# Optimization experiments

Hardware: AMD Instinct MI355X
Metric: run time of the kernel (lower is better)

The kernel has to match this reference:

```python
import jax, jax.numpy as jnp
import numpy as np

OBS, H, Z = 64, 128, 64
T, B = 512, 1024
EPS = 0.01


def _lin(x, W, b):
    # torch nn.Linear: y = x @ W.T + b, W: [out, in]
    return x @ W.T + b


def setup_inputs() -> dict:
    key = jax.random.key(0)
    ks = jax.random.split(key, 16)
    n = lambda k, shape: 0.1 * jax.random.normal(k, shape, dtype=jnp.float32)
    z = lambda shape: jnp.zeros(shape, dtype=jnp.float32)
    return {
        "s": jax.random.normal(ks[0], (T, B, OBS), dtype=jnp.float32),
        "noise": jax.random.normal(ks[1], (T, B, Z), dtype=jnp.float32),
        # phi_s / phi_z
        "W_phi_s": n(ks[2], (H, OBS)), "b_phi_s": z((H,)),
        "W_phi_z": n(ks[3], (H, Z)), "b_phi_z": z((H,)),
        # prior: Linear(H,H) ReLU Linear(H,2Z)
        "Wp1": n(ks[4], (H, H)), "bp1": z((H,)),
        "Wp2": n(ks[5], (2 * Z, H)), "bp2": z((2 * Z,)),
        # encoder: Linear(2H,H) ReLU Linear(H,2Z)
        "We1": n(ks[6], (H, 2 * H)), "be1": z((H,)),
        "We2": n(ks[7], (2 * Z, H)), "be2": z((2 * Z,)),
        # LSTMCell(input=2H, hidden=H), gate order i,f,g,o
        "W_ih": n(ks[8], (4 * H, 2 * H)), "b_ih": z((4 * H,)),
        "W_hh": n(ks[9], (4 * H, H)), "b_hh": z((4 * H,)),
        # decoder: Linear(2H,H) ReLU Linear(H,OBS)
        "Wd1": n(ks[10], (H, 2 * H)), "bd1": z((H,)),
        "Wd2": n(ks[11], (OBS, H)), "bd2": z((OBS,)),
    }


def reference(s, noise, W_phi_s, b_phi_s, W_phi_z, b_phi_z, Wp1, bp1, Wp2, bp2,
              We1, be1, We2, be2, W_ih, b_ih, W_hh, b_hh, Wd1, bd1, Wd2, bd2):
    h0 = jnp.zeros((s.shape[1], H), dtype=s.dtype)
    c0 = jnp.zeros((s.shape[1], H), dtype=s.dtype)

    def step(carry, xs):
        h, c, kl_acc, rc_acc = carry
        s_t, n_t = xs
        phi_s = _lin(s_t, W_phi_s, b_phi_s)                      # [B, H]
        # encoder on [phi_s, h]
        enc = _lin(jax.nn.relu(_lin(jnp.concatenate([phi_s, h], -1), We1, be1)), We2, be2)
        z_mu, z_std = jnp.split(enc, 2, axis=-1)
        z_std = jax.nn.softplus(z_std)
        # prior on h
        pri = _lin(jax.nn.relu(_lin(h, Wp1, bp1)), Wp2, bp2)
        p_mu, p_std = jnp.split(pri, 2, axis=-1)
        p_std = jax.nn.softplus(p_std)
        # reparameterize
        z_samp = z_mu + z_std * n_t
        phi_z = _lin(z_samp, W_phi_z, b_phi_z)                   # [B, H]
        # decode from [phi_z, h]
        recon = _lin(jax.nn.relu(_lin(jnp.concatenate([phi_z, h], -1), Wd1, bd1)), Wd2, bd2)
        # LSTM cell update with input [phi_s, phi_z]
        gates = _lin(jnp.concatenate([phi_s, phi_z], -1), W_ih, b_ih) + _lin(h, W_hh, b_hh)
        gi, gf, gg, go = jnp.split(gates, 4, axis=-1)
        c_new = jax.nn.sigmoid(gf) * c + jax.nn.sigmoid(gi) * jnp.tanh(gg)
        h_new = jax.nn.sigmoid(go) * jnp.tanh(c_new)
        # losses (sum over feature dim, mean over batch)
        rc_t = (0.5 * jnp.square(recon - s_t)).sum(-1).mean()
        kl_t = 0.5 * (2.0 * jnp.log(p_std + EPS) - 2.0 * jnp.log(z_std + EPS)
                      + (jnp.square(z_std) + jnp.square(z_mu - p_mu))
                      / (jnp.square(jnp.exp(p_std)) - 1.0)).sum(-1).mean()
        return (h_new, c_new, kl_acc + kl_t, rc_acc + rc_t), None

    (_, _, total_kl, total_rc), _ = jax.lax.scan(
        step, (h0, c0, jnp.float32(0.0), jnp.float32(0.0)), (s, noise))
    return total_kl + total_rc
```

## Files before the change

kernel.cpp:

```cpp
#include <hip/hip_runtime.h>

typedef __bf16 bf16_t;
typedef bf16_t bf16x8 __attribute__((ext_vector_type(8)));
typedef float  f32x4  __attribute__((ext_vector_type(4)));

#define TT 512
#define BB 1024

#define cL0   0
#define cL1   1024
#define cL2   3072
#define cL3   5120
#define cL4   7168
#define cL5   9216
#define cL6   10240
#define cL7   12288
#define cL8   13312
#define cL9   17408
#define cL10  21504
#define NCHUNK 29696

#define WS_FBIAS_OFF 475136
#define WS_FOLD_OFF  478208
#define WS_HSEQ_OFF  1048576
#define WS_NEED (WS_HSEQ_OFF + (size_t)TT * BB * 128 * 2)

__device__ __forceinline__ f32x4 mfma16(bf16x8 a, bf16x8 b, f32x4 c) {
  return __builtin_amdgcn_mfma_f32_16x16x32_bf16(a, b, c, 0, 0, 0);
}
__device__ __forceinline__ float sigm(float x) { return 1.0f / (1.0f + __expf(-x)); }
__device__ __forceinline__ float tanh_f(float x) {
  x = fminf(fmaxf(x, -15.0f), 15.0f);
  float e = __expf(2.0f * x);
  return (e - 1.0f) / (e + 1.0f);
}
__device__ __forceinline__ float softplus_f(float x) {
  return (x > 15.0f) ? x : __logf(1.0f + __expf(x));
}
__device__ __forceinline__ void wg_barrier() {
  asm volatile("s_waitcnt lgkmcnt(0)\n\ts_barrier" ::: "memory");
}
__device__ __forceinline__ void keep(bf16x8& v) { asm volatile("" : "+v"(v)); }

__global__ void vrnn_fold(const float* __restrict__ We1, const float* __restrict__ Wd1,
                          const float* __restrict__ Wih,
                          const float* __restrict__ Wps, const float* __restrict__ Wpz,
                          const float* __restrict__ bps, const float* __restrict__ bpz,
                          const float* __restrict__ be1, const float* __restrict__ bd1,
                          const float* __restrict__ bih, const float* __restrict__ bhh,
                          float* __restrict__ fold, float* __restrict__ fbias) {
  int id = blockIdx.x * 256 + threadIdx.x;
  if (id < 8192) {
    int n = id >> 6, k = id & 63; float acc = 0.f;
    for (int j = 0; j < 128; ++j) acc += We1[n*256 + j] * Wps[j*64 + k];
    fold[id] = acc;
  } else if (id < 16384) {
    int q = id - 8192; int n = q >> 6, k = q & 63; float acc = 0.f;
    for (int j = 0; j < 128; ++j) acc += Wd1[n*256 + j] * Wpz[j*64 + k];
    fold[id] = acc;
  } else if (id < 49152) {
    int q = id - 16384; int n = q >> 6, k = q & 63; float acc = 0.f;
    for (int j = 0; j < 128; ++j) acc += Wih[n*256 + j] * Wps[j*64 + k];
    fold[id] = acc;
  } else if (id < 81920) {
    int q = id - 49152; int n = q >> 6, k = q & 63; float acc = 0.f;
    for (int j = 0; j < 128; ++j) acc += Wih[n*256 + 128 + j] * Wpz[j*64 + k];
    fold[id] = acc;
  } else if (id < 82048) {
    int n = id - 81920; float acc = be1[n];
    for (int j = 0; j < 128; ++j) acc += We1[n*256 + j] * bps[j];
    fbias[n] = acc;
  } else if (id < 82176) {
    int n = id - 82048; float acc = bd1[n];
    for (int j = 0; j < 128; ++j) acc += Wd1[n*256 + j] * bpz[j];
    fbias[128 + n] = acc;
  } else if (id < 82688) {
    int n = id - 82176; float acc = bih[n] + bhh[n];
    for (int j = 0; j < 128; ++j) acc += Wih[n*256 + j]*bps[j] + Wih[n*256 + 128 + j]*bpz[j];
    fbias[256 + n] = acc;
  }
}

__global__ void vrnn_pack(const float* __restrict__ fold,
                          const float* __restrict__ We1, const float* __restrict__ We2,
                          const float* __restrict__ Wp1, const float* __restrict__ Wp2,
                          const float* __restrict__ Wd1, const float* __restrict__ Wd2,
                          const float* __restrict__ Whh,
                          bf16_t* __restrict__ packed) {
  int c = blockIdx.x * 256 + threadIdx.x;
  if (c >= NCHUNK) return;
  const float* src; int rs, co, Kt, base;
  if      (c < 1024)  { base = cL0;  src = fold;          rs = 64;  co = 0;   Kt = 2; }
  else if (c < 3072)  { base = cL1;  src = We1;           rs = 256; co = 128; Kt = 4; }
  else if (c < 5120)  { base = cL2;  src = We2;           rs = 128; co = 0;   Kt = 4; }
  else if (c < 7168)  { base = cL3;  src = Wp1;           rs = 128; co = 0;   Kt = 4; }
  else if (c < 9216)  { base = cL4;  src = Wp2;           rs = 128; co = 0;   Kt = 4; }
  else if (c < 10240) { base = cL5;  src = fold + 8192;   rs = 64;  co = 0;   Kt = 2; }
  else if (c < 12288) { base = cL6;  src = Wd1;           rs = 256; co = 128; Kt = 4; }
  else if (c < 13312) { base = cL7;  src = Wd2;           rs = 128; co = 0;   Kt = 4; }
  else if (c < 17408) { base = cL8;  src = fold + 16384;  rs = 64;  co = 0;   Kt = 2; }
  else if (c < 21504) { base = cL9;  src = fold + 49152;  rs = 64;  co = 0;   Kt = 2; }
  else                { base = cL10; src = Whh;           rs = 128; co = 0;   Kt = 4; }
  int local = c - base;
  int nt = local / (Kt * 64);
  int r = local - nt * Kt * 64;
  int kt = r >> 6, lane = r & 63;
  int n = nt * 16 + (lane & 15);
  int k = kt * 32 + (lane >> 4) * 8;
  const float* p = src + n * rs + co + k;
  bf16x8 v;
  #pragma unroll
  for (int j = 0; j < 8; ++j) v[j] = (bf16_t)p[j];
  *(bf16x8*)(packed + (size_t)c * 8) = v;
}

__global__ __launch_bounds__(512, 2) void vrnn_loop(
    const float* __restrict__ s, const float* __restrict__ noise,
    const bf16_t* __restrict__ packed, const float* __restrict__ fbias,
    const float* __restrict__ be2, bf16_t* __restrict__ hseq) {
  const bf16x8* Wf = (const bf16x8*)packed;

  __shared__ __align__(16) bf16_t A_h[2][16 * 136];
  __shared__ __align__(16) bf16_t A_s[2][16 * 72];
  __shared__ __align__(16) bf16_t A_z[16 * 72];
  __shared__ __align__(16) bf16_t A_e1[16 * 136];
  __shared__ __align__(16) bf16_t Wmu_lds[2048 * 8];
  __shared__ float bsm[768];

  const int tid  = threadIdx.x;
  const int wv   = tid >> 6, ln = tid & 63;
  const int quad = ln >> 4, col = ln & 15;
  const int row0 = blockIdx.x * 16;
  const int pm_  = tid >> 5;
  const int pj   = (tid & 31) * 2;
  const int nloc0 = wv * 16 + col;
  const int j_own = wv * 16 + col;
  const int wq   = wv & 3;

  for (int i = tid; i < 768; i += 512) {
    float v;
    if      (i < 128) v = fbias[i];
    else if (i < 256) v = be2[i - 128];
    else              v = fbias[256 + (i - 256)];
    bsm[i] = v;
  }
  {
    bf16x8* wl = (bf16x8*)Wmu_lds;
    for (int c = tid; c < 2048; c += 512) wl[c] = Wf[cL2 + c];
  }
  for (int i = tid; i < 16 * 136; i += 512) A_h[0][i] = (bf16_t)0.0f;
  {
    float2 v = *(const float2*)(s + ((size_t)0 * BB + row0 + pm_) * 64 + pj);
    A_s[0][pm_ * 72 + pj]     = (bf16_t)v.x;
    A_s[0][pm_ * 72 + pj + 1] = (bf16_t)v.y;
  }
  {
    unsigned long long* p = (unsigned long long*)(hseq + (size_t)row0 * 128);
    p[tid] = 0ull;
  }

  bf16x8 rb10[4][4], rb8[4][2], rb9[4][2], wE[6];
  #pragma unroll
  for (int i = 0; i < 4; ++i) {
    int nt = wv + 8 * i;
    #pragma unroll
    for (int k = 0; k < 4; ++k) { rb10[i][k] = Wf[cL10 + (nt * 4 + k) * 64 + ln]; keep(rb10[i][k]); }
    rb8[i][0] = Wf[cL8 + (nt * 2 + 0) * 64 + ln]; keep(rb8[i][0]);
    rb8[i][1] = Wf[cL8 + (nt * 2 + 1) * 64 + ln]; keep(rb8[i][1]);
    rb9[i][0] = Wf[cL9 + (nt * 2 + 0) * 64 + ln]; keep(rb9[i][0]);
    rb9[i][1] = Wf[cL9 + (nt * 2 + 1) * 64 + ln]; keep(rb9[i][1]);
  }
  wE[0] = Wf[cL0 + (wv * 2 + 0) * 64 + ln]; keep(wE[0]);
  wE[1] = Wf[cL0 + (wv * 2 + 1) * 64 + ln]; keep(wE[1]);
  #pragma unroll
  for (int k = 0; k < 4; ++k) { wE[2 + k] = Wf[cL1 + (wv * 4 + k) * 64 + ln]; keep(wE[2 + k]); }

  float nzr[4] = {0.f, 0.f, 0.f, 0.f};
  if (wv < 4) {
    #pragma unroll
    for (int r = 0; r < 4; ++r)
      nzr[r] = noise[((size_t)0 * BB + row0 + quad * 4 + r) * 64 + j_own];
  }
  float2 svN = *(const float2*)(s + ((size_t)1 * BB + row0 + pm_) * 64 + pj);

  f32x4 c_reg = {0.f, 0.f, 0.f, 0.f};
  __syncthreads();

  int cb = 0;
  for (int t = 0; t < TT; ++t) {
    const int sb = t & 1;

    bf16x8 ah0 = *(const bf16x8*)&A_h[cb][col * 136 + 0 + quad * 8];
    bf16x8 ah1 = *(const bf16x8*)&A_h[cb][col * 136 + 32 + quad * 8];
    bf16x8 ah2 = *(const bf16x8*)&A_h[cb][col * 136 + 64 + quad * 8];
    bf16x8 ah3 = *(const bf16x8*)&A_h[cb][col * 136 + 96 + quad * 8];
    bf16x8 as0 = *(const bf16x8*)&A_s[sb][col * 72 + 0 + quad * 8];
    bf16x8 as1 = *(const bf16x8*)&A_s[sb][col * 72 + 32 + quad * 8];

    {
      float bv = bsm[nloc0];
      f32x4 c = {bv, bv, bv, bv};
      c = mfma16(as0, wE[0], c);
      c = mfma16(as1, wE[1], c);
      c = mfma16(ah0, wE[2], c);
      c = mfma16(ah1, wE[3], c);
      c = mfma16(ah2, wE[4], c);
      c = mfma16(ah3, wE[5], c);
      #pragma unroll
      for (int r = 0; r < 4; ++r)
        A_e1[(quad * 4 + r) * 136 + nloc0] = (bf16_t)fmaxf(c[r], 0.0f);
    }
    f32x4 Cg[4];
    #pragma unroll
    for (int i = 0; i < 4; ++i) {
      float bv = bsm[256 + j_own + 128 * i];
      f32x4 cc = {bv, bv, bv, bv};
      cc = mfma16(ah0, rb10[i][0], cc);
      cc = mfma16(ah1, rb10[i][1], cc);
      cc = mfma16(ah2, rb10[i][2], cc);
      cc = mfma16(ah3, rb10[i][3], cc);
      cc = mfma16(as0, rb8[i][0], cc);
      cc = mfma16(as1, rb8[i][1], cc);
      Cg[i] = cc;
    }
    wg_barrier();

    {
      int lzo = 0;
      asm volatile("" : "+s"(lzo));
      const bf16x8* Wml = (const bf16x8*)Wmu_lds + lzo;
      if (wv < 4) {
        bf16x8 wmu[4], wsd[4];
        #pragma unroll
        for (int k = 0; k < 4; ++k) {
          wmu[k] = Wml[(wq * 4 + k) * 64 + ln];
          wsd[k] = Wml[((wq + 4) * 4 + k) * 64 + ln];
        }
        bf16x8 ae0 = *(const bf16x8*)&A_e1[col * 136 + 0 + quad * 8];
        bf16x8 ae1 = *(const bf16x8*)&A_e1[col * 136 + 32 + quad * 8];
        bf16x8 ae2 = *(const bf16x8*)&A_e1[col * 136 + 64 + quad * 8];
        bf16x8 ae3 = *(const bf16x8*)&A_e1[col * 136 + 96 + quad * 8];
        float bm = bsm[128 + wq * 16 + col], bs = bsm[128 + 64 + wq * 16 + col];
        f32x4 cm = {bm, bm, bm, bm};
        f32x4 cs = {bs, bs, bs, bs};
        cm = mfma16(ae0, wmu[0], cm); cs = mfma16(ae0, wsd[0], cs);
        cm = mfma16(ae1, wmu[1], cm); cs = mfma16(ae1, wsd[1], cs);
        cm = mfma16(ae2, wmu[2], cm); cs = mfma16(ae2, wsd[2], cs);
        cm = mfma16(ae3, wmu[3], cm); cs = mfma16(ae3, wsd[3], cs);
        #pragma unroll
        for (int r = 0; r < 4; ++r) {
          float z = cm[r] + softplus_f(cs[r]) * nzr[r];
          A_z[(quad * 4 + r) * 72 + wq * 16 + col] = (bf16_t)z;
        }
      }
    }
    if (t + 1 < TT) {
      A_s[sb ^ 1][pm_ * 72 + pj]     = (bf16_t)svN.x;
      A_s[sb ^ 1][pm_ * 72 + pj + 1] = (bf16_t)svN.y;
    }
    wg_barrier();

    if (wv < 4 && t + 1 < TT) {
      #pragma unroll
      for (int r = 0; r < 4; ++r)
        nzr[r] = noise[((size_t)(t + 1) * BB + row0 + quad * 4 + r) * 64 + j_own];
    }
    if (t + 2 < TT)
      svN = *(const float2*)(s + ((size_t)(t + 2) * BB + row0 + pm_) * 64 + pj);

    {
      bf16x8 az0 = *(const bf16x8*)&A_z[col * 72 + 0 + quad * 8];
      bf16x8 az1 = *(const bf16x8*)&A_z[col * 72 + 32 + quad * 8];
      #pragma unroll
      for (int i = 0; i < 4; ++i) {
        Cg[i] = mfma16(az0, rb9[i][0], Cg[i]);
        Cg[i] = mfma16(az1, rb9[i][1], Cg[i]);
      }
    }
    bf16_t* hp = hseq + (size_t)(t + 1) * BB * 128;
    #pragma unroll
    for (int r = 0; r < 4; ++r) {
      float gi = sigm(Cg[0][r]);
      float gf = sigm(Cg[1][r]);
      float gg = tanh_f(Cg[2][r]);
      float go = sigm(Cg[3][r]);
      float cn = gf * c_reg[r] + gi * gg;
      c_reg[r] = cn;
      bf16_t hv = (bf16_t)(go * tanh_f(cn));
      A_h[cb ^ 1][(quad * 4 + r) * 136 + j_own] = hv;
      if (t + 1 < TT) hp[(size_t)(row0 + quad * 4 + r) * 128 + j_own] = hv;
    }
    wg_barrier();
    cb ^= 1;
  }
}

__global__ __launch_bounds__(512, 2) void vrnn_tail(
    const float* __restrict__ s, const float* __restrict__ noise,
    const bf16_t* __restrict__ packed, const float* __restrict__ fbias,
    const float* __restrict__ bp1, const float* __restrict__ bp2,
    const float* __restrict__ be2, const float* __restrict__ bd2,
    const bf16_t* __restrict__ hseq, float* __restrict__ out) {
  const bf16x8* Wf = (const bf16x8*)packed;

  __shared__ __align__(16) bf16_t A_h[16 * 136];
  __shared__ __align__(16) bf16_t A_s[16 * 72];
  __shared__ __align__(16) bf16_t A_z[16 * 72];
  __shared__ __align__(16) bf16_t A_e1[16 * 136];
  __shared__ __align__(16) bf16_t A_p1[16 * 136];
  __shared__ __align__(16) bf16_t A_d1[16 * 136];
  __shared__ float zmu_s[16 * 68], zsd_s[16 * 68];
  __shared__ float dec2o[16 * 68];
  __shared__ float bsm[704];
  __shared__ float red[8];

  const int tid  = threadIdx.x;
  const int wv   = tid >> 6, ln = tid & 63;
  const int quad = ln >> 4, col = ln & 15;
  const int pm_  = tid >> 5;
  const int pj   = (tid & 31) * 2;
  const int nloc0 = wv * 16 + col;
  const int wq   = wv & 3;

  for (int i = tid; i < 704; i += 512) {
    float v;
    if      (i < 128) v = fbias[i];
    else if (i < 256) v = bp1[i - 128];
    else if (i < 384) v = be2[i - 256];
    else if (i < 512) v = bp2[i - 384];
    else if (i < 640) v = fbias[128 + (i - 512)];
    else              v = bd2[i - 640];
    bsm[i] = v;
  }

  bf16x8 wE[6], wP1[4], wmu[4], wsd[4], wD1[4], w5[2], w7[4];
  wE[0] = Wf[cL0 + (wv * 2 + 0) * 64 + ln];
  wE[1] = Wf[cL0 + (wv * 2 + 1) * 64 + ln];
  #pragma unroll
  for (int k = 0; k < 4; ++k) {
    wE[2 + k] = Wf[cL1 + (wv * 4 + k) * 64 + ln];
    wP1[k] = Wf[cL3 + (wv * 4 + k) * 64 + ln];
    wD1[k] = Wf[cL6 + (wv * 4 + k) * 64 + ln];
    w7[k]  = Wf[cL7 + (wq * 4 + k) * 64 + ln];
  }
  {
    int base2 = (wv < 4) ? cL2 : cL4;
    #pragma unroll
    for (int k = 0; k < 4; ++k) {
      wmu[k] = Wf[base2 + (wq * 4 + k) * 64 + ln];
      wsd[k] = Wf[base2 + ((wq + 4) * 4 + k) * 64 + ln];
    }
  }
  w5[0] = Wf[cL5 + (wv * 2 + 0) * 64 + ln];
  w5[1] = Wf[cL5 + (wv * 2 + 1) * 64 + ln];
  #pragma unroll
  for (int k = 0; k < 6; ++k) keep(wE[k]);
  #pragma unroll
  for (int k = 0; k < 4; ++k) { keep(wP1[k]); keep(wmu[k]); keep(wsd[k]); keep(wD1[k]); keep(w7[k]); }
  keep(w5[0]); keep(w5[1]);

  float kl_acc = 0.0f, rc_acc = 0.0f;
  __syncthreads();

  const int hm  = tid >> 5;
  const int hc4 = (tid & 31) * 4;

  for (int tau = blockIdx.x; tau < TT * 64; tau += gridDim.x) {
    const int t = tau >> 6;
    const int row0 = (tau & 63) * 16;

    {
      unsigned long long hv = *(const unsigned long long*)(
          hseq + (size_t)t * BB * 128 + (size_t)(row0 + hm) * 128 + hc4);
      *(unsigned long long*)&A_h[hm * 136 + hc4] = hv;
    }
    float2 sv = *(const float2*)(s + ((size_t)t * BB + row0 + pm_) * 64 + pj);
    A_s[pm_ * 72 + pj]     = (bf16_t)sv.x;
    A_s[pm_ * 72 + pj + 1] = (bf16_t)sv.y;
    float nzr[4];
    if (wv < 4) {
      #pragma unroll
      for (int r = 0; r < 4; ++r)
        nzr[r] = noise[((size_t)t * BB + row0 + quad * 4 + r) * 64 + wq * 16 + col];
    }
    wg_barrier();

    bf16x8 ah0 = *(const bf16x8*)&A_h[col * 136 + 0 + quad * 8];
    bf16x8 ah1 = *(const bf16x8*)&A_h[col * 136 + 32 + quad * 8];
    bf16x8 ah2 = *(const bf16x8*)&A_h[col * 136 + 64 + quad * 8];
    bf16x8 ah3 = *(const bf16x8*)&A_h[col * 136 + 96 + quad * 8];
    bf16x8 as0 = *(const bf16x8*)&A_s[col * 72 + 0 + quad * 8];
    bf16x8 as1 = *(const bf16x8*)&A_s[col * 72 + 32 + quad * 8];
    {
      float bv = bsm[nloc0];
      f32x4 c = {bv, bv, bv, bv};
      c = mfma16(as0, wE[0], c);
      c = mfma16(as1, wE[1], c);
      c = mfma16(ah0, wE[2], c);
      c = mfma16(ah1, wE[3], c);
      c = mfma16(ah2, wE[4], c);
      c = mfma16(ah3, wE[5], c);
      #pragma unroll
      for (int r = 0; r < 4; ++r)
        A_e1[(quad * 4 + r) * 136 + nloc0] = (bf16_t)fmaxf(c[r], 0.0f);
    }
    {
      float bv = bsm[128 + nloc0];
      f32x4 c = {bv, bv, bv, bv};
      c = mfma16(ah0, wP1[0], c);
      c = mfma16(ah1, wP1[1], c);
      c = mfma16(ah2, wP1[2], c);
      c = mfma16(ah3, wP1[3], c);
      #pragma unroll
      for (int r = 0; r < 4; ++r)
        A_p1[(quad * 4 + r) * 136 + nloc0] = (bf16_t)fmaxf(c[r], 0.0f);
    }
    wg_barrier();

    float Pmu[4], Pps[4];
    if (wv < 4) {
      bf16x8 ae0 = *(const bf16x8*)&A_e1[col * 136 + 0 + quad * 8];
      bf16x8 ae1 = *(const bf16x8*)&A_e1[col * 136 + 32 + quad * 8];
      bf16x8 ae2 = *(const bf16x8*)&A_e1[col * 136 + 64 + quad * 8];
      bf16x8 ae3 = *(const bf16x8*)&A_e1[col * 136 + 96 + quad * 8];
      float bm = bsm[256 + wq * 16 + col], bs = bsm[256 + 64 + wq * 16 + col];
      f32x4 cm = {bm, bm, bm, bm};
      f32x4 cs = {bs, bs, bs, bs};
      cm = mfma16(ae0, wmu[0], cm); cs = mfma16(ae0, wsd[0], cs);
      cm = mfma16(ae1, wmu[1], cm); cs = mfma16(ae1, wsd[1], cs);
      cm = mfma16(ae2, wmu[2], cm); cs = mfma16(ae2, wsd[2], cs);
      cm = mfma16(ae3, wmu[3], cm); cs = mfma16(ae3, wsd[3], cs);
      #pragma unroll
      for (int r = 0; r < 4; ++r) {
        float zm = cm[r];
        float zs = softplus_f(cs[r]);
        int m = quad * 4 + r;
        A_z[m * 72 + wq * 16 + col] = (bf16_t)(zm + zs * nzr[r]);
        zmu_s[m * 68 + wq * 16 + col] = zm;
        zsd_s[m * 68 + wq * 16 + col] = zs;
      }
    } else {
      bf16x8 ap0 = *(const bf16x8*)&A_p1[col * 136 + 0 + quad * 8];
      bf16x8 ap1 = *(const bf16x8*)&A_p1[col * 136 + 32 + quad * 8];
      bf16x8 ap2 = *(const bf16x8*)&A_p1[col * 136 + 64 + quad * 8];
      bf16x8 ap3 = *(const bf16x8*)&A_p1[col * 136 + 96 + quad * 8];
      float bm = bsm[384 + wq * 16 + col], bs = bsm[384 + 64 + wq * 16 + col];
      f32x4 cm = {bm, bm, bm, bm};
      f32x4 cs = {bs, bs, bs, bs};
      cm = mfma16(ap0, wmu[0], cm); cs = mfma16(ap0, wsd[0], cs);
      cm = mfma16(ap1, wmu[1], cm); cs = mfma16(ap1, wsd[1], cs);
      cm = mfma16(ap2, wmu[2], cm); cs = mfma16(ap2, wsd[2], cs);
      cm = mfma16(ap3, wmu[3], cm); cs = mfma16(ap3, wsd[3], cs);
      #pragma unroll
      for (int r = 0; r < 4; ++r) { Pmu[r] = cm[r]; Pps[r] = softplus_f(cs[r]); }
    }
    wg_barrier();

    {
      bf16x8 az0 = *(const bf16x8*)&A_z[col * 72 + 0 + quad * 8];
      bf16x8 az1 = *(const bf16x8*)&A_z[col * 72 + 32 + quad * 8];
      float bv = bsm[512 + nloc0];
      f32x4 c = {bv, bv, bv, bv};
      c = mfma16(az0, w5[0], c);
      c = mfma16(az1, w5[1], c);
      c = mfma16(ah0, wD1[0], c);
      c = mfma16(ah1, wD1[1], c);
      c = mfma16(ah2, wD1[2], c);
      c = mfma16(ah3, wD1[3], c);
      #pragma unroll
      for (int r = 0; r < 4; ++r)
        A_d1[(quad * 4 + r) * 136 + nloc0] = (bf16_t)fmaxf(c[r], 0.0f);
    }
    if (wv >= 4) {
      #pragma unroll
      for (int r = 0; r < 4; ++r) {
        int m = quad * 4 + r;
        float zm = zmu_s[m * 68 + wq * 16 + col];
        float zs = zsd_s[m * 68 + wq * 16 + col];
        float dm = zm - Pmu[r];
        float ps = Pps[r];
        float den = __expf(2.0f * ps) - 1.0f;
        kl_acc += 0.5f * (2.0f * __logf(ps + 0.01f) - 2.0f * __logf(zs + 0.01f)
                          + (zs * zs + dm * dm) / den);
      }
    }
    wg_barrier();

    if (wv >= 4) {
      bf16x8 ad0 = *(const bf16x8*)&A_d1[col * 136 + 0 + quad * 8];
      bf16x8 ad1 = *(const bf16x8*)&A_d1[col * 136 + 32 + quad * 8];
      bf16x8 ad2 = *(const bf16x8*)&A_d1[col * 136 + 64 + quad * 8];
      bf16x8 ad3 = *(const bf16x8*)&A_d1[col * 136 + 96 + quad * 8];
      float bv = bsm[640 + wq * 16 + col];
      f32x4 c = {bv, bv, bv, bv};
      c = mfma16(ad0, w7[0], c);
      c = mfma16(ad1, w7[1], c);
      c = mfma16(ad2, w7[2], c);
      c = mfma16(ad3, w7[3], c);
      #pragma unroll
      for (int r = 0; r < 4; ++r)
        dec2o[(quad * 4 + r) * 68 + wq * 16 + col] = c[r];
    }
    wg_barrier();
    {
      float d0 = dec2o[pm_ * 68 + pj] - sv.x;
      float d1 = dec2o[pm_ * 68 + pj + 1] - sv.y;
      rc_acc += 0.5f * (d0 * d0 + d1 * d1);
    }
  }

  float tot = (kl_acc + rc_acc) * (1.0f / 1024.0f);
  #pragma unroll
  for (int off = 32; off > 0; off >>= 1) tot += __shfl_down(tot, off);
  if (ln == 0) red[wv] = tot;
  __syncthreads();
  if (tid == 0) {
    float sum = 0.f;
    #pragma unroll
    for (int i = 0; i < 8; ++i) sum += red[i];
    atomicAdd(out, sum);
  }
}

__global__ __launch_bounds__(512, 2) void vrnn_mono(
    const float* __restrict__ s, const float* __restrict__ noise,
    const bf16_t* __restrict__ packed, const float* __restrict__ fbias,
    const float* __restrict__ bp1, const float* __restrict__ bp2,
    const float* __restrict__ be2, const float* __restrict__ bd2,
    float* __restrict__ out) {
  const bf16x8* Wf = (const bf16x8*)packed;
  __shared__ __align__(16) bf16_t A_h[16 * 136];
  __shared__ __align__(16) bf16_t A_s[2][16 * 72];
  __shared__ __align__(16) bf16_t A_z[16 * 72];
  __shared__ __align__(16) bf16_t A_e1[16 * 136];
  __shared__ __align__(16) bf16_t A_p1[16 * 136];
  __shared__ __align__(16) bf16_t A_d1[16 * 136];
  __shared__ float zmu_s[16 * 68], zsd_s[16 * 68];
  __shared__ float dec2o[16 * 68];
  __shared__ float bsm[1216];
  __shared__ float red[8];
  const int tid  = threadIdx.x;
  const int wv   = tid >> 6, ln = tid & 63;
  const int quad = ln >> 4, col = ln & 15;
  const int row0 = blockIdx.x * 16;
  const int pm_  = tid >> 5;
  const int pj   = (tid & 31) * 2;
  const int nloc0 = wv * 16 + col;
  const int j_own = wv * 16 + col;
  const int wq   = wv & 3;
  for (int i = tid; i < 1216; i += 512) {
    float v;
    if      (i < 128)  v = fbias[i];
    else if (i < 256)  v = bp1[i - 128];
    else if (i < 384)  v = be2[i - 256];
    else if (i < 512)  v = bp2[i - 384];
    else if (i < 640)  v = fbias[128 + (i - 512)];
    else if (i < 704)  v = bd2[i - 640];
    else               v = fbias[256 + (i - 704)];
    bsm[i] = v;
  }
  for (int i = tid; i < 16 * 136; i += 512) A_h[i] = (bf16_t)0.0f;
  {
    float2 v = *(const float2*)(s + ((size_t)0 * BB + row0 + pm_) * 64 + pj);
    A_s[0][pm_ * 72 + pj]     = (bf16_t)v.x;
    A_s[0][pm_ * 72 + pj + 1] = (bf16_t)v.y;
  }
  bf16x8 rb9[4][2], rb10[4][4];
  #pragma unroll
  for (int i = 0; i < 4; ++i) {
    int nt = wv + 8 * i;
    rb9[i][0] = Wf[cL9 + (nt * 2 + 0) * 64 + ln];
    rb9[i][1] = Wf[cL9 + (nt * 2 + 1) * 64 + ln];
    #pragma unroll
    for (int k = 0; k < 4; ++k) rb10[i][k] = Wf[cL10 + (nt * 4 + k) * 64 + ln];
  }
  bf16x8 wE0[2], wE1[4];
  wE0[0] = Wf[cL0 + (wv * 2 + 0) * 64 + ln];
  wE0[1] = Wf[cL0 + (wv * 2 + 1) * 64 + ln];
  #pragma unroll
  for (int k = 0; k < 4; ++k) wE1[k] = Wf[cL1 + (wv * 4 + k) * 64 + ln];
  bf16x8 wmu[4], wsd[4];
  {
    int base2 = (wv < 4) ? cL2 : cL4;
    #pragma unroll
    for (int k = 0; k < 4; ++k) {
      wmu[k] = Wf[base2 + (wq * 4 + k) * 64 + ln];
      wsd[k] = Wf[base2 + ((wq + 4) * 4 + k) * 64 + ln];
    }
  }
  f32x4 c_reg = {0.f, 0.f, 0.f, 0.f};
  float kl_acc = 0.0f, rc_acc = 0.0f;
  __syncthreads();
  for (int t = 0; t < TT; ++t) {
    const int sb = t & 1;
    float nzr[4];
    if (wv < 4) {
      #pragma unroll
      for (int r = 0; r < 4; ++r)
        nzr[r] = noise[((size_t)t * BB + row0 + quad * 4 + r) * 64 + j_own];
    }
    float2 svv = make_float2(0.f, 0.f);
    if (t + 1 < TT) svv = *(const float2*)(s + ((size_t)(t + 1) * BB + row0 + pm_) * 64 + pj);
    float2 spv = make_float2(0.f, 0.f);
    if (t > 0) spv = *(const float2*)(s + ((size_t)(t - 1) * BB + row0 + pm_) * 64 + pj);
    bf16x8 w8[4][2], wP1[4], wD1[4];
    #pragma unroll
    for (int i = 0; i < 4; ++i) {
      int nt = wv + 8 * i;
      w8[i][0] = Wf[cL8 + (nt * 2 + 0) * 64 + ln];
      w8[i][1] = Wf[cL8 + (nt * 2 + 1) * 64 + ln];
    }
    #pragma unroll
    for (int k = 0; k < 4; ++k) {
      wP1[k] = Wf[cL3 + (wv * 4 + k) * 64 + ln];
      wD1[k] = Wf[cL6 + (wv * 4 + k) * 64 + ln];
    }
    bf16x8 ah0 = *(const bf16x8*)&A_h[col * 136 + 0 + quad * 8];
    bf16x8 ah1 = *(const bf16x8*)&A_h[col * 136 + 32 + quad * 8];
    bf16x8 ah2 = *(const bf16x8*)&A_h[col * 136 + 64 + quad * 8];
    bf16x8 ah3 = *(const bf16x8*)&A_h[col * 136 + 96 + quad * 8];
    bf16x8 as0 = *(const bf16x8*)&A_s[sb][col * 72 + 0 + quad * 8];
    bf16x8 as1 = *(const bf16x8*)&A_s[sb][col * 72 + 32 + quad * 8];
    {
      float bv = bsm[nloc0];
      f32x4 c = {bv, bv, bv, bv};
      c = mfma16(as0, wE0[0], c);
      c = mfma16(as1, wE0[1], c);
      c = mfma16(ah0, wE1[0], c);
      c = mfma16(ah1, wE1[1], c);
      c = mfma16(ah2, wE1[2], c);
      c = mfma16(ah3, wE1[3], c);
      #pragma unroll
      for (int r = 0; r < 4; ++r)
        A_e1[(quad * 4 + r) * 136 + nloc0] = (bf16_t)fmaxf(c[r], 0.0f);
    }
    f32x4 Cg[4];
    #pragma unroll
    for (int i = 0; i < 4; ++i) {
      float bv = bsm[704 + j_own + 128 * i];
      f32x4 cc = {bv, bv, bv, bv};
      cc = mfma16(ah0, rb10[i][0], cc);
      cc = mfma16(ah1, rb10[i][1], cc);
      cc = mfma16(ah2, rb10[i][2], cc);
      cc = mfma16(ah3, rb10[i][3], cc);
      cc = mfma16(as0, w8[i][0], cc);
      cc = mfma16(as1, w8[i][1], cc);
      Cg[i] = cc;
    }
    {
      float bv = bsm[128 + nloc0];
      f32x4 c = {bv, bv, bv, bv};
      c = mfma16(ah0, wP1[0], c);
      c = mfma16(ah1, wP1[1], c);
      c = mfma16(ah2, wP1[2], c);
      c = mfma16(ah3, wP1[3], c);
      #pragma unroll
      for (int r = 0; r < 4; ++r)
        A_p1[(quad * 4 + r) * 136 + nloc0] = (bf16_t)fmaxf(c[r], 0.0f);
    }
    f32x4 Cd;
    {
      float bv = bsm[512 + nloc0];
      f32x4 c = {bv, bv, bv, bv};
      c = mfma16(ah0, wD1[0], c);
      c = mfma16(ah1, wD1[1], c);
      c = mfma16(ah2, wD1[2], c);
      c = mfma16(ah3, wD1[3], c);
      Cd = c;
    }
    if (wv >= 4 && t > 0) {
      bf16x8 ad0 = *(const bf16x8*)&A_d1[col * 136 + 0 + quad * 8];
      bf16x8 ad1 = *(const bf16x8*)&A_d1[col * 136 + 32 + quad * 8];
      bf16x8 ad2 = *(const bf16x8*)&A_d1[col * 136 + 64 + quad * 8];
      bf16x8 ad3 = *(const bf16x8*)&A_d1[col * 136 + 96 + quad * 8];
      bf16x8 w7[4];
      #pragma unroll
      for (int k = 0; k < 4; ++k) w7[k] = Wf[cL7 + (wq * 4 + k) * 64 + ln];
      float bv = bsm[640 + wq * 16 + col];
      f32x4 c = {bv, bv, bv, bv};
      c = mfma16(ad0, w7[0], c);
      c = mfma16(ad1, w7[1], c);
      c = mfma16(ad2, w7[2], c);
      c = mfma16(ad3, w7[3], c);
      #pragma unroll
      for (int r = 0; r < 4; ++r)
        dec2o[(quad * 4 + r) * 68 + wq * 16 + col] = c[r];
    }
    wg_barrier();
    float Pmu[4], Pps[4];
    if (wv < 4) {
      bf16x8 ae0 = *(const bf16x8*)&A_e1[col * 136 + 0 + quad * 8];
      bf16x8 ae1 = *(const bf16x8*)&A_e1[col * 136 + 32 + quad * 8];
      bf16x8 ae2 = *(const bf16x8*)&A_e1[col * 136 + 64 + quad * 8];
      bf16x8 ae3 = *(const bf16x8*)&A_e1[col * 136 + 96 + quad * 8];
      float bm = bsm[256 + wq * 16 + col], bs = bsm[256 + 64 + wq * 16 + col];
      f32x4 cm = {bm, bm, bm, bm};
      f32x4 cs = {bs, bs, bs, bs};
      cm = mfma16(ae0, wmu[0], cm); cs = mfma16(ae0, wsd[0], cs);
      cm = mfma16(ae1, wmu[1], cm); cs = mfma16(ae1, wsd[1], cs);
      cm = mfma16(ae2, wmu[2], cm); cs = mfma16(ae2, wsd[2], cs);
      cm = mfma16(ae3, wmu[3], cm); cs = mfma16(ae3, wsd[3], cs);
      #pragma unroll
      for (int r = 0; r < 4; ++r) {
        float zm = cm[r];
        float zs = softplus_f(cs[r]);
        float z = zm + zs * nzr[r];
        int m = quad * 4 + r;
        A_z[m * 72 + j_own] = (bf16_t)z;
        zmu_s[m * 68 + j_own] = zm;
        zsd_s[m * 68 + j_own] = zs;
      }
    } else {
      bf16x8 ap0 = *(const bf16x8*)&A_p1[col * 136 + 0 + quad * 8];
      bf16x8 ap1 = *(const bf16x8*)&A_p1[col * 136 + 32 + quad * 8];
      bf16x8 ap2 = *(const bf16x8*)&A_p1[col * 136 + 64 + quad * 8];
      bf16x8 ap3 = *(const bf16x8*)&A_p1[col * 136 + 96 + quad * 8];
      float bm = bsm[384 + wq * 16 + col], bs = bsm[384 + 64 + wq * 16 + col];
      f32x4 cm = {bm, bm, bm, bm};
      f32x4 cs = {bs, bs, bs, bs};
      cm = mfma16(ap0, wmu[0], cm); cs = mfma16(ap0, wsd[0], cs);
      cm = mfma16(ap1, wmu[1], cm); cs = mfma16(ap1, wsd[1], cs);
      cm = mfma16(ap2, wmu[2], cm); cs = mfma16(ap2, wsd[2], cs);
      cm = mfma16(ap3, wmu[3], cm); cs = mfma16(ap3, wsd[3], cs);
      #pragma unroll
      for (int r = 0; r < 4; ++r) { Pmu[r] = cm[r]; Pps[r] = softplus_f(cs[r]); }
    }
    if (t > 0) {
      float d0 = dec2o[pm_ * 68 + pj] - spv.x;
      float d1 = dec2o[pm_ * 68 + pj + 1] - spv.y;
      rc_acc += 0.5f * (d0 * d0 + d1 * d1);
    }
    if (t + 1 < TT) {
      A_s[sb ^ 1][pm_ * 72 + pj]     = (bf16_t)svv.x;
      A_s[sb ^ 1][pm_ * 72 + pj + 1] = (bf16_t)svv.y;
    }
    wg_barrier();
    bf16x8 az0 = *(const bf16x8*)&A_z[col * 72 + 0 + quad * 8];
    bf16x8 az1 = *(const bf16x8*)&A_z[col * 72 + 32 + quad * 8];
    #pragma unroll
    for (int i = 0; i < 4; ++i) {
      Cg[i] = mfma16(az0, rb9[i][0], Cg[i]);
      Cg[i] = mfma16(az1, rb9[i][1], Cg[i]);
    }
    {
      bf16x8 w5a = Wf[cL5 + (wv * 2 + 0) * 64 + ln];
      bf16x8 w5b = Wf[cL5 + (wv * 2 + 1) * 64 + ln];
      Cd = mfma16(az0, w5a, Cd);
      Cd = mfma16(az1, w5b, Cd);
      #pragma unroll
      for (int r = 0; r < 4; ++r)
        A_d1[(quad * 4 + r) * 136 + nloc0] = (bf16_t)fmaxf(Cd[r], 0.0f);
    }
    #pragma unroll
    for (int r = 0; r < 4; ++r) {
      float gi = sigm(Cg[0][r]);
      float gf = sigm(Cg[1][r]);
      float gg = tanh_f(Cg[2][r]);
      float go = sigm(Cg[3][r]);
      float cn = gf * c_reg[r] + gi * gg;
      c_reg[r] = cn;
      A_h[(quad * 4 + r) * 136 + j_own] = (bf16_t)(go * tanh_f(cn));
    }
    if (wv >= 4) {
      #pragma unroll
      for (int r = 0; r < 4; ++r) {
        int m = quad * 4 + r;
        float zm = zmu_s[m * 68 + wq * 16 + col];
        float zs = zsd_s[m * 68 + wq * 16 + col];
        float dm = zm - Pmu[r];
        float ps = Pps[r];
        float den = __expf(2.0f * ps) - 1.0f;
        kl_acc += 0.5f * (2.0f * __logf(ps + 0.01f) - 2.0f * __logf(zs + 0.01f)
                          + (zs * zs + dm * dm) / den);
      }
    }
    wg_barrier();
  }
  if (wv >= 4) {
    bf16x8 ad0 = *(const bf16x8*)&A_d1[col * 136 + 0 + quad * 8];
    bf16x8 ad1 = *(const bf16x8*)&A_d1[col * 136 + 32 + quad * 8];
    bf16x8 ad2 = *(const bf16x8*)&A_d1[col * 136 + 64 + quad * 8];
    bf16x8 ad3 = *(const bf16x8*)&A_d1[col * 136 + 96 + quad * 8];
    bf16x8 w7[4];
    #pragma unroll
    for (int k = 0; k < 4; ++k) w7[k] = Wf[cL7 + (wq * 4 + k) * 64 + ln];
    float bv = bsm[640 + wq * 16 + col];
    f32x4 c = {bv, bv, bv, bv};
    c = mfma16(ad0, w7[0], c);
    c = mfma16(ad1, w7[1], c);
    c = mfma16(ad2, w7[2], c);
    c = mfma16(ad3, w7[3], c);
    #pragma unroll
    for (int r = 0; r < 4; ++r)
      dec2o[(quad * 4 + r) * 68 + wq * 16 + col] = c[r];
  }
  __syncthreads();
  {
    float2 sl = *(const float2*)(s + ((size_t)(TT - 1) * BB + row0 + pm_) * 64 + pj);
    float d0 = dec2o[pm_ * 68 + pj] - sl.x;
    float d1 = dec2o[pm_ * 68 + pj + 1] - sl.y;
    rc_acc += 0.5f * (d0 * d0 + d1 * d1);
  }
  float tot = (kl_acc + rc_acc) * (1.0f / 1024.0f);
  #pragma unroll
  for (int off = 32; off > 0; off >>= 1) tot += __shfl_down(tot, off);
  if (ln == 0) red[wv] = tot;
  __syncthreads();
  if (tid == 0) {
    float sum = 0.f;
    #pragma unroll
    for (int i = 0; i < 8; ++i) sum += red[i];
    atomicAdd(out, sum);
  }
}

extern "C" void kernel_launch(void* const* d_in, const int* in_sizes, int n_in,
                              void* d_out, int out_size, void* d_ws, size_t ws_size,
                              hipStream_t stream) {
  (void)in_sizes; (void)n_in; (void)out_size;
  const float* s   = (const float*)d_in[0];
  const float* nz  = (const float*)d_in[1];
  const float* Wps = (const float*)d_in[2];
  const float* bps = (const float*)d_in[3];
  const float* Wpz = (const float*)d_in[4];
  const float* bpz = (const float*)d_in[5];
  const float* Wp1 = (const float*)d_in[6];
  const float* bp1 = (const float*)d_in[7];
  const float* Wp2 = (const float*)d_in[8];
  const float* bp2 = (const float*)d_in[9];
  const float* We1 = (const float*)d_in[10];
  const float* be1 = (const float*)d_in[11];
  const float* We2 = (const float*)d_in[12];
  const float* be2 = (const float*)d_in[13];
  const float* Wih = (const float*)d_in[14];
  const float* bih = (const float*)d_in[15];
  const float* Whh = (const float*)d_in[16];
  const float* bhh = (const float*)d_in[17];
  const float* Wd1 = (const float*)d_in[18];
  const float* bd1 = (const float*)d_in[19];
  const float* Wd2 = (const float*)d_in[20];
  const float* bd2 = (const float*)d_in[21];

  bf16_t* packed = (bf16_t*)d_ws;
  float* fbias = (float*)((char*)d_ws + WS_FBIAS_OFF);
  float* fold  = (float*)((char*)d_ws + WS_FOLD_OFF);
  bf16_t* hseq = (bf16_t*)((char*)d_ws + WS_HSEQ_OFF);

  hipMemsetAsync(d_out, 0, sizeof(float), stream);
  vrnn_fold<<<(82688 + 255) / 256, 256, 0, stream>>>(We1, Wd1, Wih, Wps, Wpz, bps, bpz,
                                                     be1, bd1, bih, bhh, fold, fbias);
  vrnn_pack<<<(NCHUNK + 255) / 256, 256, 0, stream>>>(fold, We1, We2, Wp1, Wp2, Wd1, Wd2,
                                                      Whh, packed);
  if (ws_size >= WS_NEED) {
    vrnn_loop<<<64, 512, 0, stream>>>(s, nz, packed, fbias, be2, hseq);
    vrnn_tail<<<256, 512, 0, stream>>>(s, nz, packed, fbias, bp1, bp2, be2, bd2, hseq,
                                       (float*)d_out);
  } else {
    vrnn_mono<<<64, 512, 0, stream>>>(s, nz, packed, fbias, bp1, bp2, be2, bd2,
                                      (float*)d_out);
  }
}
```

Before: 1.868 ms.

## Fuse recurrent loop and loss tail into single monolithic kernel with register-resident weights

Replaces the two-kernel split, a recurrent LSTM loop that writes every hidden state to a workspace followed by a parallel tail kernel that recomputes encoder, prior and decoder losses, with one kernel that does all per-step work inside the recurrence. Prior, decoder and second-layer weights are kept in registers or LDS, and the recon loss is pipelined one step late to hide the decoder's second layer. This removes the hidden-state write and reload traffic and the second launch. In exchange it adds MFMA and LDS work to the serial critical path of the 64-block recurrence, and raises register and LDS pressure.

```diff
diff --git a/kernel.cpp b/kernel.cpp
--- a/kernel.cpp
+++ b/kernel.cpp
@@ -22,8 +22,6 @@
 
 #define WS_FBIAS_OFF 475136
 #define WS_FOLD_OFF  478208
-#define WS_HSEQ_OFF  1048576
-#define WS_NEED (WS_HSEQ_OFF + (size_t)TT * BB * 128 * 2)
 
 __device__ __forceinline__ f32x4 mfma16(bf16x8 a, bf16x8 b, f32x4 c) {
   return __builtin_amdgcn_mfma_f32_16x16x32_bf16(a, b, c, 0, 0, 0);
@@ -114,18 +112,25 @@
   *(bf16x8*)(packed + (size_t)c * 8) = v;
 }
 
-__global__ __launch_bounds__(512, 2) void vrnn_loop(
+__global__ __launch_bounds__(512, 2) void vrnn_mono2(
     const float* __restrict__ s, const float* __restrict__ noise,
     const bf16_t* __restrict__ packed, const float* __restrict__ fbias,
-    const float* __restrict__ be2, bf16_t* __restrict__ hseq) {
+    const float* __restrict__ bp1, const float* __restrict__ bp2,
+    const float* __restrict__ be2, const float* __restrict__ bd2,
+    float* __restrict__ out) {
   const bf16x8* Wf = (const bf16x8*)packed;
 
   __shared__ __align__(16) bf16_t A_h[2][16 * 136];
   __shared__ __align__(16) bf16_t A_s[2][16 * 72];
   __shared__ __align__(16) bf16_t A_z[16 * 72];
   __shared__ __align__(16) bf16_t A_e1[16 * 136];
-  __shared__ __align__(16) bf16_t Wmu_lds[2048 * 8];
-  __shared__ float bsm[768];
+  __shared__ __align__(16) bf16_t A_p1[16 * 136];
+  __shared__ __align__(16) bf16_t A_d1[16 * 136];
+  __shared__ __align__(16) bf16_t Wlds[4096 * 8];
+  __shared__ float zmu_s[16 * 68], zsd_s[16 * 68];
+  __shared__ float dec2o[16 * 68];
+  __shared__ float bsm[1216];
+  __shared__ float red[8];
 
   const int tid  = threadIdx.x;
   const int wv   = tid >> 6, ln = tid & 63;
@@ -137,29 +142,25 @@
   const int j_own = wv * 16 + col;
   const int wq   = wv & 3;
 
-  for (int i = tid; i < 768; i += 512) {
+  for (int i = tid; i < 1216; i += 512) {
     float v;
-    if      (i < 128) v = fbias[i];
-    else if (i < 256) v = be2[i - 128];
-    else              v = fbias[256 + (i - 256)];
+    if      (i < 128)  v = fbias[i];
+    else if (i < 256)  v = bp1[i - 128];
+    else if (i < 384)  v = be2[i - 256];
+    else if (i < 512)  v = bp2[i - 384];
+    else if (i < 640)  v = fbias[128 + (i - 512)];
+    else if (i < 704)  v = bd2[i - 640];
+    else               v = fbias[256 + (i - 704)];
     bsm[i] = v;
   }
   {
-    bf16x8* wl = (bf16x8*)Wmu_lds;
-    for (int c = tid; c < 2048; c += 512) wl[c] = Wf[cL2 + c];
+    bf16x8* wl = (bf16x8*)Wlds;
+    for (int c = tid; c < 4096; c += 512)
+      wl[c] = Wf[(c < 2048) ? (cL2 + c) : (cL4 + (c - 2048))];
   }
   for (int i = tid; i < 16 * 136; i += 512) A_h[0][i] = (bf16_t)0.0f;
-  {
-    float2 v = *(const float2*)(s + ((size_t)0 * BB + row0 + pm_) * 64 + pj);
-    A_s[0][pm_ * 72 + pj]     = (bf16_t)v.x;
-    A_s[0][pm_ * 72 + pj + 1] = (bf16_t)v.y;
-  }
-  {
-    unsigned long long* p = (unsigned long long*)(hseq + (size_t)row0 * 128);
-    p[tid] = 0ull;
-  }
-
-  bf16x8 rb10[4][4], rb8[4][2], rb9[4][2], wE[6];
+
+  bf16x8 rb10[4][4], rb8[4][2], rb9[4][2], wE[6], wP1[4], wD1[4], w5[2], w7[4];
   #pragma unroll
   for (int i = 0; i < 4; ++i) {
     int nt = wv + 8 * i;
@@ -173,7 +174,14 @@
   wE[0] = Wf[cL0 + (wv * 2 + 0) * 64 + ln]; keep(wE[0]);
   wE[1] = Wf[cL0 + (wv * 2 + 1) * 64 + ln]; keep(wE[1]);
   #pragma unroll
-  for (int k = 0; k < 4; ++k) { wE[2 + k] = Wf[cL1 + (wv * 4 + k) * 64 + ln]; keep(wE[2 + k]); }
+  for (int k = 0; k < 4; ++k) {
+    wE[2 + k] = Wf[cL1 + (wv * 4 + k) * 64 + ln]; keep(wE[2 + k]);
+    wP1[k] = Wf[cL3 + (wv * 4 + k) * 64 + ln]; keep(wP1[k]);
+    wD1[k] = Wf[cL6 + (wv * 4 + k) * 64 + ln]; keep(wD1[k]);
+    w7[k]  = Wf[cL7 + (wq * 4 + k) * 64 + ln]; keep(w7[k]);
+  }
+  w5[0] = Wf[cL5 + (wv * 2 + 0) * 64 + ln]; keep(w5[0]);
+  w5[1] = Wf[cL5 + (wv * 2 + 1) * 64 + ln]; keep(w5[1]);
 
   float nzr[4] = {0.f, 0.f, 0.f, 0.f};
   if (wv < 4) {
@@ -181,9 +189,16 @@
     for (int r = 0; r < 4; ++r)
       nzr[r] = noise[((size_t)0 * BB + row0 + quad * 4 + r) * 64 + j_own];
   }
+  float2 sP0 = *(const float2*)(s + ((size_t)0 * BB + row0 + pm_) * 64 + pj);
   float2 svN = *(const float2*)(s + ((size_t)1 * BB + row0 + pm_) * 64 + pj);
+  float2 sPm1 = make_float2(0.f, 0.f);
+  {
+    A_s[0][pm_ * 72 + pj]     = (bf16_t)sP0.x;
+    A_s[0][pm_ * 72 + pj + 1] = (bf16_t)sP0.y;
+  }
 
   f32x4 c_reg = {0.f, 0.f, 0.f, 0.f};
+  float kl_acc = 0.0f, rc_acc = 0.0f;
   __syncthreads();
 
   int cb = 0;
@@ -210,10 +225,31 @@
       for (int r = 0; r < 4; ++r)
         A_e1[(quad * 4 + r) * 136 + nloc0] = (bf16_t)fmaxf(c[r], 0.0f);
     }
+    {
+      float bv = bsm[128 + nloc0];
+      f32x4 c = {bv, bv, bv, bv};
+      c = mfma16(ah0, wP1[0], c);
+      c = mfma16(ah1, wP1[1], c);
+      c = mfma16(ah2, wP1[2], c);
+      c = mfma16(ah3, wP1[3], c);
+      #pragma unroll
+      for (int r = 0; r < 4; ++r)
+        A_p1[(quad * 4 + r) * 136 + nloc0] = (bf16_t)fmaxf(c[r], 0.0f);
+    }
+    f32x4 Cd;
+    {
+      float bv = bsm[512 + nloc0];
+      f32x4 c = {bv, bv, bv, bv};
+      c = mfma16(ah0, wD1[0], c);
+      c = mfma16(ah1, wD1[1], c);
+      c = mfma16(ah2, wD1[2], c);
+      c = mfma16(ah3, wD1[3], c);
+      Cd = c;
+    }
     f32x4 Cg[4];
     #pragma unroll
     for (int i = 0; i < 4; ++i) {
-      float bv = bsm[256 + j_own + 128 * i];
+      float bv = bsm[704 + j_own + 128 * i];
       f32x4 cc = {bv, bv, bv, bv};
       cc = mfma16(ah0, rb10[i][0], cc);
       cc = mfma16(ah1, rb10[i][1], cc);
@@ -223,24 +259,40 @@
       cc = mfma16(as1, rb8[i][1], cc);
       Cg[i] = cc;
     }
+    if (wv >= 4 && t > 0) {
+      bf16x8 ad0 = *(const bf16x8*)&A_d1[col * 136 + 0 + quad * 8];
+      bf16x8 ad1 = *(const bf16x8*)&A_d1[col * 136 + 32 + quad * 8];
+      bf16x8 ad2 = *(const bf16x8*)&A_d1[col * 136 + 64 + quad * 8];
+      bf16x8 ad3 = *(const bf16x8*)&A_d1[col * 136 + 96 + quad * 8];
+      float bv = bsm[640 + wq * 16 + col];
+      f32x4 c = {bv, bv, bv, bv};
+      c = mfma16(ad0, w7[0], c);
+      c = mfma16(ad1, w7[1], c);
+      c = mfma16(ad2, w7[2], c);
+      c = mfma16(ad3, w7[3], c);
+      #pragma unroll
+      for (int r = 0; r < 4; ++r)
+        dec2o[(quad * 4 + r) * 68 + wq * 16 + col] = c[r];
+    }
     wg_barrier();
 
+    float Pmu[4], Pps[4];
     {
       int lzo = 0;
       asm volatile("" : "+s"(lzo));
-      const bf16x8* Wml = (const bf16x8*)Wmu_lds + lzo;
+      const bf16x8* Wml = (const bf16x8*)Wlds + ((wv < 4) ? 0 : 2048) + lzo;
+      bf16x8 wmu[4], wsd[4];
+      #pragma unroll
+      for (int k = 0; k < 4; ++k) {
+        wmu[k] = Wml[(wq * 4 + k) * 64 + ln];
+        wsd[k] = Wml[((wq + 4) * 4 + k) * 64 + ln];
+      }
       if (wv < 4) {
-        bf16x8 wmu[4], wsd[4];
-        #pragma unroll
-        for (int k = 0; k < 4; ++k) {
-          wmu[k] = Wml[(wq * 4 + k) * 64 + ln];
-          wsd[k] = Wml[((wq + 4) * 4 + k) * 64 + ln];
-        }
         bf16x8 ae0 = *(const bf16x8*)&A_e1[col * 136 + 0 + quad * 8];
         bf16x8 ae1 = *(const bf16x8*)&A_e1[col * 136 + 32 + quad * 8];
         bf16x8 ae2 = *(const bf16x8*)&A_e1[col * 136 + 64 + quad * 8];
         bf16x8 ae3 = *(const bf16x8*)&A_e1[col * 136 + 96 + quad * 8];
-        float bm = bsm[128 + wq * 16 + col], bs = bsm[128 + 64 + wq * 16 + col];
+        float bm = bsm[256 + wq * 16 + col], bs = bsm[256 + 64 + wq * 16 + col];
         f32x4 cm = {bm, bm, bm, bm};
         f32x4 cs = {bs, bs, bs, bs};
         cm = mfma16(ae0, wmu[0], cm); cs = mfma16(ae0, wsd[0], cs);
@@ -249,15 +301,40 @@
         cm = mfma16(ae3, wmu[3], cm); cs = mfma16(ae3, wsd[3], cs);
         #pragma unroll
         for (int r = 0; r < 4; ++r) {
-          float z = cm[r] + softplus_f(cs[r]) * nzr[r];
-          A_z[(quad * 4 + r) * 72 + wq * 16 + col] = (bf16_t)z;
+          float zm = cm[r];
+          float zs = softplus_f(cs[r]);
+          int m = quad * 4 + r;
+          A_z[m * 72 + wq * 16 + col] = (bf16_t)(zm + zs * nzr[r]);
+          zmu_s[m * 68 + wq * 16 + col] = zm;
+          zsd_s[m * 68 + wq * 16 + col] = zs;
         }
+      } else {
+        bf16x8 ap0 = *(const bf16x8*)&A_p1[col * 136 + 0 + quad * 8];
+        bf16x8 ap1 = *(const bf16x8*)&A_p1[col * 136 + 32 + quad * 8];
+        bf16x8 ap2 = *(const bf16x8*)&A_p1[col * 136 + 64 + quad * 8];
+        bf16x8 ap3 = *(const bf16x8*)&A_p1[col * 136 + 96 + quad * 8];
+        float bm = bsm[384 + wq * 16 + col], bs = bsm[384 + 64 + wq * 16 + col];
+        f32x4 cm = {bm, bm, bm, bm};
+        f32x4 cs = {bs, bs, bs, bs};
+        cm = mfma16(ap0, wmu[0], cm); cs = mfma16(ap0, wsd[0], cs);
+        cm = mfma16(ap1, wmu[1], cm); cs = mfma16(ap1, wsd[1], cs);
+        cm = mfma16(ap2, wmu[2], cm); cs = mfma16(ap2, wsd[2], cs);
+        cm = mfma16(ap3, wmu[3], cm); cs = mfma16(ap3, wsd[3], cs);
+        #pragma unroll
+        for (int r = 0; r < 4; ++r) { Pmu[r] = cm[r]; Pps[r] = softplus_f(cs[r]); }
       }
+    }
+    if (t > 0) {
+      float d0 = dec2o[pm_ * 68 + pj] - sPm1.x;
+      float d1 = dec2o[pm_ * 68 + pj + 1] - sPm1.y;
+      rc_acc += 0.5f * (d0 * d0 + d1 * d1);
     }
     if (t + 1 < TT) {
       A_s[sb ^ 1][pm_ * 72 + pj]     = (bf16_t)svN.x;
       A_s[sb ^ 1][pm_ * 72 + pj + 1] = (bf16_t)svN.y;
     }
+    sPm1 = sP0;
+    sP0 = svN;
     wg_barrier();
 
     if (wv < 4 && t + 1 < TT) {
@@ -276,8 +353,12 @@
         Cg[i] = mfma16(az0, rb9[i][0], Cg[i]);
         Cg[i] = mfma16(az1, rb9[i][1], Cg[i]);
       }
-    }
-    bf16_t* hp = hseq + (size_t)(t + 1) * BB * 128;
+      Cd = mfma16(az0, w5[0], Cd);
+      Cd = mfma16(az1, w5[1], Cd);
+      #pragma unroll
+      for (int r = 0; r < 4; ++r)
+        A_d1[(quad * 4 + r) * 136 + nloc0] = (bf16_t)fmaxf(Cd[r], 0.0f);
+    }
     #pragma unroll
     for (int r = 0; r < 4; ++r) {
       float gi = sigm(Cg[0][r]);
@@ -286,190 +367,7 @@
       float go = sigm(Cg[3][r]);
       float cn = gf * c_reg[r] + gi * gg;
       c_reg[r] = cn;
-      bf16_t hv = (bf16_t)(go * tanh_f(cn));
-      A_h[cb ^ 1][(quad * 4 + r) * 136 + j_own] = hv;
-      if (t + 1 < TT) hp[(size_t)(row0 + quad * 4 + r) * 128 + j_own] = hv;
-    }
-    wg_barrier();
-    cb ^= 1;
-  }
-}
-
-__global__ __launch_bounds__(512, 2) void vrnn_tail(
-    const float* __restrict__ s, const float* __restrict__ noise,
-    const bf16_t* __restrict__ packed, const float* __restrict__ fbias,
-    const float* __restrict__ bp1, const float* __restrict__ bp2,
-    const float* __restrict__ be2, const float* __restrict__ bd2,
-    const bf16_t* __restrict__ hseq, float* __restrict__ out) {
-  const bf16x8* Wf = (const bf16x8*)packed;
-
-  __shared__ __align__(16) bf16_t A_h[16 * 136];
-  __shared__ __align__(16) bf16_t A_s[16 * 72];
-  __shared__ __align__(16) bf16_t A_z[16 * 72];
-  __shared__ __align__(16) bf16_t A_e1[16 * 136];
-  __shared__ __align__(16) bf16_t A_p1[16 * 136];
-  __shared__ __align__(16) bf16_t A_d1[16 * 136];
-  __shared__ float zmu_s[16 * 68], zsd_s[16 * 68];
-  __shared__ float dec2o[16 * 68];
-  __shared__ float bsm[704];
-  __shared__ float red[8];
-
-  const int tid  = threadIdx.x;
-  const int wv   = tid >> 6, ln = tid & 63;
-  const int quad = ln >> 4, col = ln & 15;
-  const int pm_  = tid >> 5;
-  const int pj   = (tid & 31) * 2;
-  const int nloc0 = wv * 16 + col;
-  const int wq   = wv & 3;
-
-  for (int i = tid; i < 704; i += 512) {
-    float v;
-    if      (i < 128) v = fbias[i];
-    else if (i < 256) v = bp1[i - 128];
-    else if (i < 384) v = be2[i - 256];
-    else if (i < 512) v = bp2[i - 384];
-    else if (i < 640) v = fbias[128 + (i - 512)];
-    else              v = bd2[i - 640];
-    bsm[i] = v;
-  }
-
-  bf16x8 wE[6], wP1[4], wmu[4], wsd[4], wD1[4], w5[2], w7[4];
-  wE[0] = Wf[cL0 + (wv * 2 + 0) * 64 + ln];
-  wE[1] = Wf[cL0 + (wv * 2 + 1) * 64 + ln];
-  #pragma unroll
-  for (int k = 0; k < 4; ++k) {
-    wE[2 + k] = Wf[cL1 + (wv * 4 + k) * 64 + ln];
-    wP1[k] = Wf[cL3 + (wv * 4 + k) * 64 + ln];
-    wD1[k] = Wf[cL6 + (wv * 4 + k) * 64 + ln];
-    w7[k]  = Wf[cL7 + (wq * 4 + k) * 64 + ln];
-  }
-  {
-    int base2 = (wv < 4) ? cL2 : cL4;
-    #pragma unroll
-    for (int k = 0; k < 4; ++k) {
-      wmu[k] = Wf[base2 + (wq * 4 + k) * 64 + ln];
-      wsd[k] = Wf[base2 + ((wq + 4) * 4 + k) * 64 + ln];
-    }
-  }
-  w5[0] = Wf[cL5 + (wv * 2 + 0) * 64 + ln];
-  w5[1] = Wf[cL5 + (wv * 2 + 1) * 64 + ln];
-  #pragma unroll
-  for (int k = 0; k < 6; ++k) keep(wE[k]);
-  #pragma unroll
-  for (int k = 0; k < 4; ++k) { keep(wP1[k]); keep(wmu[k]); keep(wsd[k]); keep(wD1[k]); keep(w7[k]); }
-  keep(w5[0]); keep(w5[1]);
-
-  float kl_acc = 0.0f, rc_acc = 0.0f;
-  __syncthreads();
-
-  const int hm  = tid >> 5;
-  const int hc4 = (tid & 31) * 4;
-
-  for (int tau = blockIdx.x; tau < TT * 64; tau += gridDim.x) {
-    const int t = tau >> 6;
-    const int row0 = (tau & 63) * 16;
-
-    {
-      unsigned long long hv = *(const unsigned long long*)(
-          hseq + (size_t)t * BB * 128 + (size_t)(row0 + hm) * 128 + hc4);
-      *(unsigned long long*)&A_h[hm * 136 + hc4] = hv;
-    }
-    float2 sv = *(const float2*)(s + ((size_t)t * BB + row0 + pm_) * 64 + pj);
-    A_s[pm_ * 72 + pj]     = (bf16_t)sv.x;
-    A_s[pm_ * 72 + pj + 1] = (bf16_t)sv.y;
-    float nzr[4];
-    if (wv < 4) {
-      #pragma unroll
-      for (int r = 0; r < 4; ++r)
-        nzr[r] = noise[((size_t)t * BB + row0 + quad * 4 + r) * 64 + wq * 16 + col];
-    }
-    wg_barrier();
-
-    bf16x8 ah0 = *(const bf16x8*)&A_h[col * 136 + 0 + quad * 8];
-    bf16x8 ah1 = *(const bf16x8*)&A_h[col * 136 + 32 + quad * 8];
-    bf16x8 ah2 = *(const bf16x8*)&A_h[col * 136 + 64 + quad * 8];
-    bf16x8 ah3 = *(const bf16x8*)&A_h[col * 136 + 96 + quad * 8];
-    bf16x8 as0 = *(const bf16x8*)&A_s[col * 72 + 0 + quad * 8];
-    bf16x8 as1 = *(const bf16x8*)&A_s[col * 72 + 32 + quad * 8];
-    {
-      float bv = bsm[nloc0];
-      f32x4 c = {bv, bv, bv, bv};
-      c = mfma16(as0, wE[0], c);
-      c = mfma16(as1, wE[1], c);
-      c = mfma16(ah0, wE[2], c);
-      c = mfma16(ah1, wE[3], c);
-      c = mfma16(ah2, wE[4], c);
-      c = mfma16(ah3, wE[5], c);
-      #pragma unroll
-      for (int r = 0; r < 4; ++r)
-        A_e1[(quad * 4 + r) * 136 + nloc0] = (bf16_t)fmaxf(c[r], 0.0f);
-    }
-    {
-      float bv = bsm[128 + nloc0];
-      f32x4 c = {bv, bv, bv, bv};
-      c = mfma16(ah0, wP1[0], c);
-      c = mfma16(ah1, wP1[1], c);
-      c = mfma16(ah2, wP1[2], c);
-      c = mfma16(ah3, wP1[3], c);
-      #pragma unroll
-      for (int r = 0; r < 4; ++r)
-        A_p1[(quad * 4 + r) * 136 + nloc0] = (bf16_t)fmaxf(c[r], 0.0f);
-    }
-    wg_barrier();
-
-    float Pmu[4], Pps[4];
-    if (wv < 4) {
-      bf16x8 ae0 = *(const bf16x8*)&A_e1[col * 136 + 0 + quad * 8];
-      bf16x8 ae1 = *(const bf16x8*)&A_e1[col * 136 + 32 + quad * 8];
-      bf16x8 ae2 = *(const bf16x8*)&A_e1[col * 136 + 64 + quad * 8];
-      bf16x8 ae3 = *(const bf16x8*)&A_e1[col * 136 + 96 + quad * 8];
-      float bm = bsm[256 + wq * 16 + col], bs = bsm[256 + 64 + wq * 16 + col];
-      f32x4 cm = {bm, bm, bm, bm};
-      f32x4 cs = {bs, bs, bs, bs};
-      cm = mfma16(ae0, wmu[0], cm); cs = mfma16(ae0, wsd[0], cs);
-      cm = mfma16(ae1, wmu[1], cm); cs = mfma16(ae1, wsd[1], cs);
-      cm = mfma16(ae2, wmu[2], cm); cs = mfma16(ae2, wsd[2], cs);
-      cm = mfma16(ae3, wmu[3], cm); cs = mfma16(ae3, wsd[3], cs);
-      #pragma unroll
-      for (int r = 0; r < 4; ++r) {
-        float zm = cm[r];
-        float zs = softplus_f(cs[r]);
-        int m = quad * 4 + r;
-        A_z[m * 72 + wq * 16 + col] = (bf16_t)(zm + zs * nzr[r]);
-        zmu_s[m * 68 + wq * 16 + col] = zm;
-        zsd_s[m * 68 + wq * 16 + col] = zs;
-      }
-    } else {
-      bf16x8 ap0 = *(const bf16x8*)&A_p1[col * 136 + 0 + quad * 8];
-      bf16x8 ap1 = *(const bf16x8*)&A_p1[col * 136 + 32 + quad * 8];
-      bf16x8 ap2 = *(const bf16x8*)&A_p1[col * 136 + 64 + quad * 8];
-      bf16x8 ap3 = *(const bf16x8*)&A_p1[col * 136 + 96 + quad * 8];
-      float bm = bsm[384 + wq * 16 + col], bs = bsm[384 + 64 + wq * 16 + col];
-      f32x4 cm = {bm, bm, bm, bm};
-      f32x4 cs = {bs, bs, bs, bs};
-      cm = mfma16(ap0, wmu[0], cm); cs = mfma16(ap0, wsd[0], cs);
-      cm = mfma16(ap1, wmu[1], cm); cs = mfma16(ap1, wsd[1], cs);
-      cm = mfma16(ap2, wmu[2], cm); cs = mfma16(ap2, wsd[2], cs);
-      cm = mfma16(ap3, wmu[3], cm); cs = mfma16(ap3, wsd[3], cs);
-      #pragma unroll
-      for (int r = 0; r < 4; ++r) { Pmu[r] = cm[r]; Pps[r] = softplus_f(cs[r]); }
-    }
-    wg_barrier();
-
-    {
-      bf16x8 az0 = *(const bf16x8*)&A_z[col * 72 + 0 + quad * 8];
-      bf16x8 az1 = *(const bf16x8*)&A_z[col * 72 + 32 + quad * 8];
-      float bv = bsm[512 + nloc0];
-      f32x4 c = {bv, bv, bv, bv};
-      c = mfma16(az0, w5[0], c);
-      c = mfma16(az1, w5[1], c);
-      c = mfma16(ah0, wD1[0], c);
-      c = mfma16(ah1, wD1[1], c);
-      c = mfma16(ah2, wD1[2], c);
-      c = mfma16(ah3, wD1[3], c);
-      #pragma unroll
-      for (int r = 0; r < 4; ++r)
-        A_d1[(quad * 4 + r) * 136 + nloc0] = (bf16_t)fmaxf(c[r], 0.0f);
+      A_h[cb ^ 1][(quad * 4 + r) * 136 + j_own] = (bf16_t)(go * tanh_f(cn));
     }
     if (wv >= 4) {
       #pragma unroll
@@ -485,28 +383,29 @@
       }
     }
     wg_barrier();
-
-    if (wv >= 4) {
-      bf16x8 ad0 = *(const bf16x8*)&A_d1[col * 136 + 0 + quad * 8];
-      bf16x8 ad1 = *(const bf16x8*)&A_d1[col * 136 + 32 + quad * 8];
-      bf16x8 ad2 = *(const bf16x8*)&A_d1[col * 136 + 64 + quad * 8];
-      bf16x8 ad3 = *(const bf16x8*)&A_d1[col * 136 + 96 + quad * 8];
-      float bv = bsm[640 + wq * 16 + col];
-      f32x4 c = {bv, bv, bv, bv};
-      c = mfma16(ad0, w7[0], c);
-      c = mfma16(ad1, w7[1], c);
-      c = mfma16(ad2, w7[2], c);
-      c = mfma16(ad3, w7[3], c);
-      #pragma unroll
-      for (int r = 0; r < 4; ++r)
-        dec2o[(quad * 4 + r) * 68 + wq * 16 + col] = c[r];
-    }
-    wg_barrier();
-    {
-      float d0 = dec2o[pm_ * 68 + pj] - sv.x;
-      float d1 = dec2o[pm_ * 68 + pj + 1] - sv.y;
-      rc_acc += 0.5f * (d0 * d0 + d1 * d1);
-    }
+    cb ^= 1;
+  }
+
+  if (wv >= 4) {
+    bf16x8 ad0 = *(const bf16x8*)&A_d1[col * 136 + 0 + quad * 8];
+    bf16x8 ad1 = *(const bf16x8*)&A_d1[col * 136 + 32 + quad * 8];
+    bf16x8 ad2 = *(const bf16x8*)&A_d1[col * 136 + 64 + quad * 8];
+    bf16x8 ad3 = *(const bf16x8*)&A_d1[col * 136 + 96 + quad * 8];
+    float bv = bsm[640 + wq * 16 + col];
+    f32x4 c = {bv, bv, bv, bv};
+    c = mfma16(ad0, w7[0], c);
+    c = mfma16(ad1, w7[1], c);
+    c = mfma16(ad2, w7[2], c);
+    c = mfma16(ad3, w7[3], c);
+    #pragma unroll
+    for (int r = 0; r < 4; ++r)
+      dec2o[(quad * 4 + r) * 68 + wq * 16 + col] = c[r];
+  }
+  wg_barrier();
+  {
+    float d0 = dec2o[pm_ * 68 + pj] - sPm1.x;
+    float d1 = dec2o[pm_ * 68 + pj + 1] - sPm1.y;
+    rc_acc += 0.5f * (d0 * d0 + d1 * d1);
   }
 
   float tot = (kl_acc + rc_acc) * (1.0f / 1024.0f);
@@ -522,302 +421,10 @@
   }
 }
 
-__global__ __launch_bounds__(512, 2) void vrnn_mono(
-    const float* __restrict__ s, const float* __restrict__ noise,
-    const bf16_t* __restrict__ packed, const float* __restrict__ fbias,
-    const float* __restrict__ bp1, const float* __restrict__ bp2,
-    const float* __restrict__ be2, const float* __restrict__ bd2,
-    float* __restrict__ out) {
-  const bf16x8* Wf = (const bf16x8*)packed;
-  __shared__ __align__(16) bf16_t A_h[16 * 136];
-  __shared__ __align__(16) bf16_t A_s[2][16 * 72];
-  __shared__ __align__(16) bf16_t A_z[16 * 72];
-  __shared__ __align__(16) bf16_t A_e1[16 * 136];
-  __shared__ __align__(16) bf16_t A_p1[16 * 136];
-  __shared__ __align__(16) bf16_t A_d1[16 * 136];
-  __shared__ float zmu_s[16 * 68], zsd_s[16 * 68];
-  __shared__ float dec2o[16 * 68];
-  __shared__ float bsm[1216];
-  __shared__ float red[8];
-  const int tid  = threadIdx.x;
-  const int wv   = tid >> 6, ln = tid & 63;
-  const int quad = ln >> 4, col = ln & 15;
-  const int row0 = blockIdx.x * 16;
-  const int pm_  = tid >> 5;
-  const int pj   = (tid & 31) * 2;
-  const int nloc0 = wv * 16 + col;
-  const int j_own = wv * 16 + col;
-  const int wq   = wv & 3;
-  for (int i = tid; i < 1216; i += 512) {
-    float v;
-    if      (i < 128)  v = fbias[i];
-    else if (i < 256)  v = bp1[i - 128];
-    else if (i < 384)  v = be2[i - 256];
-    else if (i < 512)  v = bp2[i - 384];
-    else if (i < 640)  v = fbias[128 + (i - 512)];
-    else if (i < 704)  v = bd2[i - 640];
-    else               v = fbias[256 + (i - 704)];
-    bsm[i] = v;
-  }
-  for (int i = tid; i < 16 * 136; i += 512) A_h[i] = (bf16_t)0.0f;
-  {
-    float2 v = *(const float2*)(s + ((size_t)0 * BB + row0 + pm_) * 64 + pj);
-    A_s[0][pm_ * 72 + pj]     = (bf16_t)v.x;
-    A_s[0][pm_ * 72 + pj + 1] = (bf16_t)v.y;
-  }
-  bf16x8 rb9[4][2], rb10[4][4];
-  #pragma unroll
-  for (int i = 0; i < 4; ++i) {
-    int nt = wv + 8 * i;
-    rb9[i][0] = Wf[cL9 + (nt * 2 + 0) * 64 + ln];
-    rb9[i][1] = Wf[cL9 + (nt * 2 + 1) * 64 + ln];
-    #pragma unroll
-    for (int k = 0; k < 4; ++k) rb10[i][k] = Wf[cL10 + (nt * 4 + k) * 64 + ln];
-  }
-  bf16x8 wE0[2], wE1[4];
-  wE0[0] = Wf[cL0 + (wv * 2 + 0) * 64 + ln];
-  wE0[1] = Wf[cL0 + (wv * 2 + 1) * 64 + ln];
-  #pragma unroll
-  for (int k = 0; k < 4; ++k) wE1[k] = Wf[cL1 + (wv * 4 + k) * 64 + ln];
-  bf16x8 wmu[4], wsd[4];
-  {
-    int base2 = (wv < 4) ? cL2 : cL4;
-    #pragma unroll
-    for (int k = 0; k < 4; ++k) {
-      wmu[k] = Wf[base2 + (wq * 4 + k) * 64 + ln];
-      wsd[k] = Wf[base2 + ((wq + 4) * 4 + k) * 64 + ln];
-    }
-  }
-  f32x4 c_reg = {0.f, 0.f, 0.f, 0.f};
-  float kl_acc = 0.0f, rc_acc = 0.0f;
-  __syncthreads();
-  for (int t = 0; t < TT; ++t) {
-    const int sb = t & 1;
-    float nzr[4];
-    if (wv < 4) {
-      #pragma unroll
-      for (int r = 0; r < 4; ++r)
-        nzr[r] = noise[((size_t)t * BB + row0 + quad * 4 + r) * 64 + j_own];
-    }
-    float2 svv = make_float2(0.f, 0.f);
-    if (t + 1 < TT) svv = *(const float2*)(s + ((size_t)(t + 1) * BB + row0 + pm_) * 64 + pj);
-    float2 spv = make_float2(0.f, 0.f);
-    if (t > 0) spv = *(const float2*)(s + ((size_t)(t - 1) * BB + row0 + pm_) * 64 + pj);
-    bf16x8 w8[4][2], wP1[4], wD1[4];
-    #pragma unroll
-    for (int i = 0; i < 4; ++i) {
-      int nt = wv + 8 * i;
-      w8[i][0] = Wf[cL8 + (nt * 2 + 0) * 64 + ln];
-      w8[i][1] = Wf[cL8 + (nt * 2 + 1) * 64 + ln];
-    }
-    #pragma unroll
-    for (int k = 0; k < 4; ++k) {
-      wP1[k] = Wf[cL3 + (wv * 4 + k) * 64 + ln];
-      wD1[k] = Wf[cL6 + (wv * 4 + k) * 64 + ln];
-    }
-    bf16x8 ah0 = *(const bf16x8*)&A_h[col * 136 + 0 + quad * 8];
-    bf16x8 ah1 = *(const bf16x8*)&A_h[col * 136 + 32 + quad * 8];
-    bf16x8 ah2 = *(const bf16x8*)&A_h[col * 136 + 64 + quad * 8];
-    bf16x8 ah3 = *(const bf16x8*)&A_h[col * 136 + 96 + quad * 8];
-    bf16x8 as0 = *(const bf16x8*)&A_s[sb][col * 72 + 0 + quad * 8];
-    bf16x8 as1 = *(const bf16x8*)&A_s[sb][col * 72 + 32 + quad * 8];
-    {
-      float bv = bsm[nloc0];
-      f32x4 c = {bv, bv, bv, bv};
-      c = mfma16(as0, wE0[0], c);
-      c = mfma16(as1, wE0[1], c);
-      c = mfma16(ah0, wE1[0], c);
-      c = mfma16(ah1, wE1[1], c);
-      c = mfma16(ah2, wE1[2], c);
-      c = mfma16(ah3, wE1[3], c);
-      #pragma unroll
-      for (int r = 0; r < 4; ++r)
-        A_e1[(quad * 4 + r) * 136 + nloc0] = (bf16_t)fmaxf(c[r], 0.0f);
-    }
-    f32x4 Cg[4];
-    #pragma unroll
-    for (int i = 0; i < 4; ++i) {
-      float bv = bsm[704 + j_own + 128 * i];
-      f32x4 cc = {bv, bv, bv, bv};
-      cc = mfma16(ah0, rb10[i][0], cc);
-      cc = mfma16(ah1, rb10[i][1], cc);
-      cc = mfma16(ah2, rb10[i][2], cc);
-      cc = mfma16(ah3, rb10[i][3], cc);
-      cc = mfma16(as0, w8[i][0], cc);
-      cc = mfma16(as1, w8[i][1], cc);
-      Cg[i] = cc;
-    }
-    {
-      float bv = bsm[128 + nloc0];
-      f32x4 c = {bv, bv, bv, bv};
-      c = mfma16(ah0, wP1[0], c);
-      c = mfma16(ah1, wP1[1], c);
-      c = mfma16(ah2, wP1[2], c);
-      c = mfma16(ah3, wP1[3], c);
-      #pragma unroll
-      for (int r = 0; r < 4; ++r)
-        A_p1[(quad * 4 + r) * 136 + nloc0] = (bf16_t)fmaxf(c[r], 0.0f);
-    }
-    f32x4 Cd;
-    {
-      float bv = bsm[512 + nloc0];
-      f32x4 c = {bv, bv, bv, bv};
-      c = mfma16(ah0, wD1[0], c);
-      c = mfma16(ah1, wD1[1], c);
-      c = mfma16(ah2, wD1[2], c);
-      c = mfma16(ah3, wD1[3], c);
-      Cd = c;
-    }
-    if (wv >= 4 && t > 0) {
-      bf16x8 ad0 = *(const bf16x8*)&A_d1[col * 136 + 0 + quad * 8];
-      bf16x8 ad1 = *(const bf16x8*)&A_d1[col * 136 + 32 + quad * 8];
-      bf16x8 ad2 = *(const bf16x8*)&A_d1[col * 136 + 64 + quad * 8];
-      bf16x8 ad3 = *(const bf16x8*)&A_d1[col * 136 + 96 + quad * 8];
-      bf16x8 w7[4];
-      #pragma unroll
-      for (int k = 0; k < 4; ++k) w7[k] = Wf[cL7 + (wq * 4 + k) * 64 + ln];
-      float bv = bsm[640 + wq * 16 + col];
-      f32x4 c = {bv, bv, bv, bv};
-      c = mfma16(ad0, w7[0], c);
-      c = mfma16(ad1, w7[1], c);
-      c = mfma16(ad2, w7[2], c);
-      c = mfma16(ad3, w7[3], c);
-      #pragma unroll
-      for (int r = 0; r < 4; ++r)
-        dec2o[(quad * 4 + r) * 68 + wq * 16 + col] = c[r];
-    }
-    wg_barrier();
-    float Pmu[4], Pps[4];
-    if (wv < 4) {
-      bf16x8 ae0 = *(const bf16x8*)&A_e1[col * 136 + 0 + quad * 8];
-      bf16x8 ae1 = *(const bf16x8*)&A_e1[col * 136 + 32 + quad * 8];
-      bf16x8 ae2 = *(const bf16x8*)&A_e1[col * 136 + 64 + quad * 8];
-      bf16x8 ae3 = *(const bf16x8*)&A_e1[col * 136 + 96 + quad * 8];
-      float bm = bsm[256 + wq * 16 + col], bs = bsm[256 + 64 + wq * 16 + col];
-      f32x4 cm = {bm, bm, bm, bm};
-      f32x4 cs = {bs, bs, bs, bs};
-      cm = mfma16(ae0, wmu[0], cm); cs = mfma16(ae0, wsd[0], cs);
-      cm = mfma16(ae1, wmu[1], cm); cs = mfma16(ae1, wsd[1], cs);
-      cm = mfma16(ae2, wmu[2], cm); cs = mfma16(ae2, wsd[2], cs);
-      cm = mfma16(ae3, wmu[3], cm); cs = mfma16(ae3, wsd[3], cs);
-      #pragma unroll
-      for (int r = 0; r < 4; ++r) {
-        float zm = cm[r];
-        float zs = softplus_f(cs[r]);
-        float z = zm + zs * nzr[r];
-        int m = quad * 4 + r;
-        A_z[m * 72 + j_own] = (bf16_t)z;
-        zmu_s[m * 68 + j_own] = zm;
-        zsd_s[m * 68 + j_own] = zs;
-      }
-    } else {
-      bf16x8 ap0 = *(const bf16x8*)&A_p1[col * 136 + 0 + quad * 8];
-      bf16x8 ap1 = *(const bf16x8*)&A_p1[col * 136 + 32 + quad * 8];
-      bf16x8 ap2 = *(const bf16x8*)&A_p1[col * 136 + 64 + quad * 8];
-      bf16x8 ap3 = *(const bf16x8*)&A_p1[col * 136 + 96 + quad * 8];
-      float bm = bsm[384 + wq * 16 + col], bs = bsm[384 + 64 + wq * 16 + col];
-      f32x4 cm = {bm, bm, bm, bm};
-      f32x4 cs = {bs, bs, bs, bs};
-      cm = mfma16(ap0, wmu[0], cm); cs = mfma16(ap0, wsd[0], cs);
-      cm = mfma16(ap1, wmu[1], cm); cs = mfma16(ap1, wsd[1], cs);
-      cm = mfma16(ap2, wmu[2], cm); cs = mfma16(ap2, wsd[2], cs);
-      cm = mfma16(ap3, wmu[3], cm); cs = mfma16(ap3, wsd[3], cs);
-      #pragma unroll
-      for (int r = 0; r < 4; ++r) { Pmu[r] = cm[r]; Pps[r] = softplus_f(cs[r]); }
-    }
-    if (t > 0) {
-      float d0 = dec2o[pm_ * 68 + pj] - spv.x;
-      float d1 = dec2o[pm_ * 68 + pj + 1] - spv.y;
-      rc_acc += 0.5f * (d0 * d0 + d1 * d1);
-    }
-    if (t + 1 < TT) {
-      A_s[sb ^ 1][pm_ * 72 + pj]     = (bf16_t)svv.x;
-      A_s[sb ^ 1][pm_ * 72 + pj + 1] = (bf16_t)svv.y;
-    }
-    wg_barrier();
-    bf16x8 az0 = *(const bf16x8*)&A_z[col * 72 + 0 + quad * 8];
-    bf16x8 az1 = *(const bf16x8*)&A_z[col * 72 + 32 + quad * 8];
-    #pragma unroll
-    for (int i = 0; i < 4; ++i) {
-      Cg[i] = mfma16(az0, rb9[i][0], Cg[i]);
-      Cg[i] = mfma16(az1, rb9[i][1], Cg[i]);
-    }
-    {
-      bf16x8 w5a = Wf[cL5 + (wv * 2 + 0) * 64 + ln];
-      bf16x8 w5b = Wf[cL5 + (wv * 2 + 1) * 64 + ln];
-      Cd = mfma16(az0, w5a, Cd);
-      Cd = mfma16(az1, w5b, Cd);
-      #pragma unroll
-      for (int r = 0; r < 4; ++r)
-        A_d1[(quad * 4 + r) * 136 + nloc0] = (bf16_t)fmaxf(Cd[r], 0.0f);
-    }
-    #pragma unroll
-    for (int r = 0; r < 4; ++r) {
-      float gi = sigm(Cg[0][r]);
-      float gf = sigm(Cg[1][r]);
-      float gg = tanh_f(Cg[2][r]);
-      float go = sigm(Cg[3][r]);
-      float cn = gf * c_reg[r] + gi * gg;
-      c_reg[r] = cn;
-      A_h[(quad * 4 + r) * 136 + j_own] = (bf16_t)(go * tanh_f(cn));
-    }
-    if (wv >= 4) {
-      #pragma unroll
-      for (int r = 0; r < 4; ++r) {
-        int m = quad * 4 + r;
-        float zm = zmu_s[m * 68 + wq * 16 + col];
-        float zs = zsd_s[m * 68 + wq * 16 + col];
-        float dm = zm - Pmu[r];
-        float ps = Pps[r];
-        float den = __expf(2.0f * ps) - 1.0f;
-        kl_acc += 0.5f * (2.0f * __logf(ps + 0.01f) - 2.0f * __logf(zs + 0.01f)
-                          + (zs * zs + dm * dm) / den);
-      }
-    }
-    wg_barrier();
-  }
-  if (wv >= 4) {
-    bf16x8 ad0 = *(const bf16x8*)&A_d1[col * 136 + 0 + quad * 8];
-    bf16x8 ad1 = *(const bf16x8*)&A_d1[col * 136 + 32 + quad * 8];
-    bf16x8 ad2 = *(const bf16x8*)&A_d1[col * 136 + 64 + quad * 8];
-    bf16x8 ad3 = *(const bf16x8*)&A_d1[col * 136 + 96 + quad * 8];
-    bf16x8 w7[4];
-    #pragma unroll
-    for (int k = 0; k < 4; ++k) w7[k] = Wf[cL7 + (wq * 4 + k) * 64 + ln];
-    float bv = bsm[640 + wq * 16 + col];
-    f32x4 c = {bv, bv, bv, bv};
-    c = mfma16(ad0, w7[0], c);
-    c = mfma16(ad1, w7[1], c);
-    c = mfma16(ad2, w7[2], c);
-    c = mfma16(ad3, w7[3], c);
-    #pragma unroll
-    for (int r = 0; r < 4; ++r)
-      dec2o[(quad * 4 + r) * 68 + wq * 16 + col] = c[r];
-  }
-  __syncthreads();
-  {
-    float2 sl = *(const float2*)(s + ((size_t)(TT - 1) * BB + row0 + pm_) * 64 + pj);
-    float d0 = dec2o[pm_ * 68 + pj] - sl.x;
-    float d1 = dec2o[pm_ * 68 + pj + 1] - sl.y;
-    rc_acc += 0.5f * (d0 * d0 + d1 * d1);
-  }
-  float tot = (kl_acc + rc_acc) * (1.0f / 1024.0f);
-  #pragma unroll
-  for (int off = 32; off > 0; off >>= 1) tot += __shfl_down(tot, off);
-  if (ln == 0) red[wv] = tot;
-  __syncthreads();
-  if (tid == 0) {
-    float sum = 0.f;
-    #pragma unroll
-    for (int i = 0; i < 8; ++i) sum += red[i];
-    atomicAdd(out, sum);
-  }
-}
-
 extern "C" void kernel_launch(void* const* d_in, const int* in_sizes, int n_in,
                               void* d_out, int out_size, void* d_ws, size_t ws_size,
                               hipStream_t stream) {
-  (void)in_sizes; (void)n_in; (void)out_size;
+  (void)in_sizes; (void)n_in; (void)out_size; (void)ws_size;
   const float* s   = (const float*)d_in[0];
   const float* nz  = (const float*)d_in[1];
   const float* Wps = (const float*)d_in[2];
@@ -844,19 +451,12 @@
   bf16_t* packed = (bf16_t*)d_ws;
   float* fbias = (float*)((char*)d_ws + WS_FBIAS_OFF);
   float* fold  = (float*)((char*)d_ws + WS_FOLD_OFF);
-  bf16_t* hseq = (bf16_t*)((char*)d_ws + WS_HSEQ_OFF);
 
   hipMemsetAsync(d_out, 0, sizeof(float), stream);
   vrnn_fold<<<(82688 + 255) / 256, 256, 0, stream>>>(We1, Wd1, Wih, Wps, Wpz, bps, bpz,
                                                      be1, bd1, bih, bhh, fold, fbias);
   vrnn_pack<<<(NCHUNK + 255) / 256, 256, 0, stream>>>(fold, We1, We2, Wp1, Wp2, Wd1, Wd2,
                                                       Whh, packed);
-  if (ws_size >= WS_NEED) {
-    vrnn_loop<<<64, 512, 0, stream>>>(s, nz, packed, fbias, be2, hseq);
-    vrnn_tail<<<256, 512, 0, stream>>>(s, nz, packed, fbias, bp1, bp2, be2, bd2, hseq,
-                                       (float*)d_out);
-  } else {
-    vrnn_mono<<<64, 512, 0, stream>>>(s, nz, packed, fbias, bp1, bp2, be2, bd2,
-                                      (float*)d_out);
-  }
-}
+  vrnn_mono2<<<64, 512, 0, stream>>>(s, nz, packed, fbias, bp1, bp2, be2, bd2,
+                                     (float*)d_out);
+}
```

After: 4.300 ms. 2.3x slower.
